# Optimization experiments

Hardware: AMD Instinct MI355X
Metric: run time of the kernel (lower is better)

Reference implementation:

```python
import jax, jax.numpy as jnp
import numpy as np

NUM_GROUPS = 8


def setup_inputs() -> dict:
    key = jax.random.key(0)
    k1, k2, k3, k4 = jax.random.split(key, 4)
    N, D_IN, D_OUT = 16384, 2048, 2048
    x = jax.random.normal(k1, (N, D_IN), dtype=jnp.float32)
    # kaiming-uniform-ish scale for weight, uniform bound for bias (values only need realistic scale)
    bound_w = 1.0 / np.sqrt(D_IN)
    weight = jax.random.uniform(k2, (NUM_GROUPS, D_OUT, D_IN), minval=-bound_w, maxval=bound_w, dtype=jnp.float32)
    bias = jax.random.uniform(k3, (NUM_GROUPS, D_OUT), minval=-bound_w, maxval=bound_w, dtype=jnp.float32)
    group_indices = jnp.sort(jax.random.randint(k4, (N,), 0, NUM_GROUPS, dtype=jnp.int32))
    return {"x": x, "weight": weight, "bias": bias, "group_indices": group_indices}


def reference(x, weight, bias, group_indices):
    """Grouped linear: out[n] = x[n] @ weight[g[n]].T + bias[g[n]].

    group_indices is sorted, so this matches the torch fallback's
    per-group gather + linear + concat row order exactly.
    """
    num_groups = weight.shape[0]
    out = jnp.zeros((x.shape[0], weight.shape[1]), dtype=x.dtype)
    for g in range(num_groups):  # fixed small loop over experts
        sel = (group_indices == g)[:, None]  # [N,1]
        # one dense GEMM per group, masked accumulate (rows not in group contribute 0)
        yg = jnp.matmul(x, weight[g].T) + bias[g]
        out = out + jnp.where(sel, yg, jnp.zeros((), dtype=x.dtype))
    return out
```

## Files before the change

kernel.cpp:

```cpp
#include <hip/hip_runtime.h>
#include <stdint.h>

#define N_ROWS 16384
#define K_DIM  2048
#define N_OUT  2048
#define NGROUPS 8
#define BM 128
#define BN 128
#define BK 32
#define MAX_Y 136

typedef short s16x8 __attribute__((ext_vector_type(8)));
typedef float f32x4 __attribute__((ext_vector_type(4)));

__device__ __forceinline__ unsigned short f2bf(float f) {
    unsigned int u = __float_as_uint(f);
    u += 0x7fffu + ((u >> 16) & 1u);
    return (unsigned short)(u >> 16);
}

__global__ void convert_kernel(const float* __restrict__ src,
                               unsigned short* __restrict__ dst, int n) {
    int stride = gridDim.x * blockDim.x;
    for (int i = blockIdx.x * blockDim.x + threadIdx.x; i * 4 < n; i += stride) {
        float4 v = *(const float4*)(src + (size_t)i * 4);
        ushort4 o;
        o.x = f2bf(v.x); o.y = f2bf(v.y); o.z = f2bf(v.z); o.w = f2bf(v.w);
        *(ushort4*)(dst + (size_t)i * 4) = o;
    }
}

__device__ __forceinline__ int lower_bound_g(const int* __restrict__ gi, int g) {
    int lo = 0, hi = N_ROWS;
    while (lo < hi) { int mid = (lo + hi) >> 1; if (gi[mid] < g) lo = mid + 1; else hi = mid; }
    return lo;
}

#define GLDS16(gp, lp) \
    __builtin_amdgcn_global_load_lds((__attribute__((address_space(1))) void*)(gp), \
                                     (__attribute__((address_space(3))) void*)(lp), 16, 0, 0)

__global__ __launch_bounds__(256) void grouped_gemm(
    const unsigned short* __restrict__ xb,
    const unsigned short* __restrict__ wb,
    const float* __restrict__ bias,
    const int* __restrict__ gi,
    float* __restrict__ out)
{
    int s[NGROUPS + 1];
    s[0] = 0; s[NGROUPS] = N_ROWS;
    #pragma unroll
    for (int g = 1; g < NGROUPS; g++) s[g] = lower_bound_g(gi, g);

    int by = blockIdx.y;
    int row0 = -1, g = 0, nrows = 0, c = 0;
    #pragma unroll
    for (int gg = 0; gg < NGROUPS; gg++) {
        int n = s[gg + 1] - s[gg];
        int tiles = (n + BM - 1) / BM;
        if (row0 < 0 && by < c + tiles) {
            g = gg;
            row0 = s[gg] + (by - c) * BM;
            nrows = n - (by - c) * BM; if (nrows > BM) nrows = BM;
        }
        c += tiles;
    }
    if (row0 < 0) return;
    int col0 = blockIdx.x * BN;

    __shared__ unsigned short As[BM * BK];
    __shared__ unsigned short Bs[BN * BK];

    int t = threadIdx.x;
    int w = t >> 6, l = t & 63;
    int la = l & 15, quad = l >> 4;
    int wm = w >> 1, wn = w & 1;

    int arow = w * 16 + (l >> 2);
    int kcol = (l & 3) * 8;
    int ar0 = min(row0 + arow,      N_ROWS - 1);
    int ar1 = min(row0 + 64 + arow, N_ROWS - 1);
    const unsigned short* gA0 = xb + (size_t)ar0 * K_DIM + kcol;
    const unsigned short* gA1 = xb + (size_t)ar1 * K_DIM + kcol;
    const unsigned short* gB0 = wb + ((size_t)g * N_OUT + col0 + arow) * K_DIM + kcol;
    const unsigned short* gB1 = gB0 + (size_t)64 * K_DIM;
    unsigned short* lA = As + w * 512;
    unsigned short* lB = Bs + w * 512;

    f32x4 acc[4][4];
    #pragma unroll
    for (int i = 0; i < 4; i++)
        #pragma unroll
        for (int j = 0; j < 4; j++)
            acc[i][j] = (f32x4){0.f, 0.f, 0.f, 0.f};

    for (int k0 = 0; k0 < K_DIM; k0 += BK) {
        GLDS16(gA0 + k0, lA);
        GLDS16(gA1 + k0, lA + 2048);
        GLDS16(gB0 + k0, lB);
        GLDS16(gB1 + k0, lB + 2048);
        __syncthreads();

        s16x8 af[4], bf_[4];
        #pragma unroll
        for (int mi = 0; mi < 4; mi++)
            af[mi] = *(const s16x8*)&As[(wm * 64 + mi * 16 + la) * BK + quad * 8];
        #pragma unroll
        for (int ni = 0; ni < 4; ni++)
            bf_[ni] = *(const s16x8*)&Bs[(wn * 64 + ni * 16 + la) * BK + quad * 8];

        #pragma unroll
        for (int mi = 0; mi < 4; mi++)
            #pragma unroll
            for (int ni = 0; ni < 4; ni++)
                acc[mi][ni] = __builtin_amdgcn_mfma_f32_16x16x32_bf16(
                    af[mi], bf_[ni], acc[mi][ni], 0, 0, 0);
        __syncthreads();
    }

    int row_end = row0 + nrows;
    float bv[4];
    #pragma unroll
    for (int ni = 0; ni < 4; ni++)
        bv[ni] = bias[g * N_OUT + col0 + wn * 64 + ni * 16 + la];
    #pragma unroll
    for (int mi = 0; mi < 4; mi++) {
        int rbase = row0 + wm * 64 + mi * 16 + quad * 4;
        #pragma unroll
        for (int r = 0; r < 4; r++) {
            int row = rbase + r;
            if (row < row_end) {
                float* op = out + (size_t)row * N_OUT + col0 + wn * 64 + la;
                #pragma unroll
                for (int ni = 0; ni < 4; ni++)
                    op[ni * 16] = acc[mi][ni][r] + bv[ni];
            }
        }
    }
}

__global__ void naive_kernel(const float* __restrict__ x, const float* __restrict__ wgt,
                             const float* __restrict__ bias, const int* __restrict__ gi,
                             float* __restrict__ out) {
    int row = blockIdx.x;
    int g = gi[row] & (NGROUPS - 1);
    __shared__ float xs[K_DIM];
    for (int i = threadIdx.x; i < K_DIM; i += 256) xs[i] = x[(size_t)row * K_DIM + i];
    __syncthreads();
    for (int c = threadIdx.x; c < N_OUT; c += 256) {
        const float* wr = wgt + ((size_t)g * N_OUT + c) * K_DIM;
        float s = 0.f;
        for (int k = 0; k < K_DIM; k++) s += xs[k] * wr[k];
        out[(size_t)row * N_OUT + c] = s + bias[g * N_OUT + c];
    }
}

extern "C" void kernel_launch(void* const* d_in, const int* in_sizes, int n_in,
                              void* d_out, int out_size, void* d_ws, size_t ws_size,
                              hipStream_t stream) {
    const float* x    = (const float*)d_in[0];
    const float* wgt  = (const float*)d_in[1];
    const float* bias = (const float*)d_in[2];
    const int*   gi   = (const int*)d_in[3];
    float* out = (float*)d_out;

    const size_t xb_bytes = (size_t)N_ROWS * K_DIM * 2;
    const size_t wb_bytes = (size_t)NGROUPS * N_OUT * K_DIM * 2;
    const size_t need = xb_bytes + wb_bytes;

    if (ws_size < need) {
        naive_kernel<<<dim3(N_ROWS), dim3(256), 0, stream>>>(x, wgt, bias, gi, out);
        return;
    }

    unsigned short* xb = (unsigned short*)d_ws;
    unsigned short* wb = (unsigned short*)((char*)d_ws + xb_bytes);

    convert_kernel<<<dim3(8192), dim3(256), 0, stream>>>(x,   xb, N_ROWS * K_DIM);
    convert_kernel<<<dim3(8192), dim3(256), 0, stream>>>(wgt, wb, NGROUPS * N_OUT * K_DIM);
    grouped_gemm<<<dim3(N_OUT / BN, MAX_Y), dim3(256), 0, stream>>>(
        xb, wb, bias, gi, out);
}
```

Baseline: 525.9 us.

## Rewrite grouped GEMM with 256x256x64 tiles, double-buffered swizzled LDS pipeline

```diff
diff --git a/kernel.cpp b/kernel.cpp
--- a/kernel.cpp
+++ b/kernel.cpp
@@ -5,10 +5,10 @@
 #define K_DIM  2048
 #define N_OUT  2048
 #define NGROUPS 8
-#define BM 128
-#define BN 128
-#define BK 32
-#define MAX_Y 136
+#define BM 256
+#define BN 256
+#define BK 64
+#define MAX_Y 72
 
 typedef short s16x8 __attribute__((ext_vector_type(8)));
 typedef float f32x4 __attribute__((ext_vector_type(4)));
@@ -40,27 +40,36 @@
     __builtin_amdgcn_global_load_lds((__attribute__((address_space(1))) void*)(gp), \
                                      (__attribute__((address_space(3))) void*)(lp), 16, 0, 0)
 
-__global__ __launch_bounds__(256) void grouped_gemm(
+#define VMW(N)  asm volatile("s_waitcnt vmcnt(" #N ")" ::: "memory")
+#define BAR()   asm volatile("s_barrier" ::: "memory")
+#define LGKM0() do { asm volatile("s_waitcnt lgkmcnt(0)" ::: "memory"); \
+                     __builtin_amdgcn_sched_barrier(0); } while (0)
+
+__global__ __launch_bounds__(512, 2) void grouped_gemm(
     const unsigned short* __restrict__ xb,
     const unsigned short* __restrict__ wb,
     const float* __restrict__ bias,
     const int* __restrict__ gi,
     float* __restrict__ out)
 {
-    int s[NGROUPS + 1];
-    s[0] = 0; s[NGROUPS] = N_ROWS;
-    #pragma unroll
-    for (int g = 1; g < NGROUPS; g++) s[g] = lower_bound_g(gi, g);
+    __shared__ unsigned char lds[131072];
+    __shared__ int sh_s[NGROUPS + 1];
+
+    const int t5 = threadIdx.x;
+
+    if (t5 <= NGROUPS)
+        sh_s[t5] = (t5 == 0) ? 0 : (t5 == NGROUPS ? N_ROWS : lower_bound_g(gi, t5));
+    __syncthreads();
 
     int by = blockIdx.y;
     int row0 = -1, g = 0, nrows = 0, c = 0;
     #pragma unroll
     for (int gg = 0; gg < NGROUPS; gg++) {
-        int n = s[gg + 1] - s[gg];
-        int tiles = (n + BM - 1) / BM;
+        int n = sh_s[gg + 1] - sh_s[gg];
+        int tiles = (n + BM - 1) >> 8;
         if (row0 < 0 && by < c + tiles) {
             g = gg;
-            row0 = s[gg] + (by - c) * BM;
+            row0 = sh_s[gg] + (by - c) * BM;
             nrows = n - (by - c) * BM; if (nrows > BM) nrows = BM;
         }
         c += tiles;
@@ -68,55 +77,80 @@
     if (row0 < 0) return;
     int col0 = blockIdx.x * BN;
 
-    __shared__ unsigned short As[BM * BK];
-    __shared__ unsigned short Bs[BN * BK];
-
-    int t = threadIdx.x;
-    int w = t >> 6, l = t & 63;
-    int la = l & 15, quad = l >> 4;
-    int wm = w >> 1, wn = w & 1;
-
-    int arow = w * 16 + (l >> 2);
-    int kcol = (l & 3) * 8;
-    int ar0 = min(row0 + arow,      N_ROWS - 1);
-    int ar1 = min(row0 + 64 + arow, N_ROWS - 1);
-    const unsigned short* gA0 = xb + (size_t)ar0 * K_DIM + kcol;
-    const unsigned short* gA1 = xb + (size_t)ar1 * K_DIM + kcol;
-    const unsigned short* gB0 = wb + ((size_t)g * N_OUT + col0 + arow) * K_DIM + kcol;
-    const unsigned short* gB1 = gB0 + (size_t)64 * K_DIM;
-    unsigned short* lA = As + w * 512;
-    unsigned short* lB = Bs + w * 512;
-
-    f32x4 acc[4][4];
-    #pragma unroll
-    for (int i = 0; i < 4; i++)
+    int rsub = t5 >> 2;
+    int swz  = (t5 & 3) ^ ((rsub >> 1) & 3);
+    int ar0 = min(row0 + rsub,       N_ROWS - 1);
+    int ar1 = min(row0 + 128 + rsub, N_ROWS - 1);
+    const unsigned short* srcA0 = xb + (size_t)ar0 * K_DIM + swz * 8;
+    const unsigned short* srcA1 = xb + (size_t)ar1 * K_DIM + swz * 8;
+    const unsigned short* srcB0 = wb + ((size_t)g * N_OUT + col0 + rsub) * K_DIM + swz * 8;
+    const unsigned short* srcB1 = srcB0 + (size_t)128 * K_DIM;
+    char* ldsA = (char*)lds;
+    char* ldsB = (char*)lds + 65536;
+    char* dA = ldsA + t5 * 16;
+    char* dB = ldsB + t5 * 16;
+
+#define STAGE_A(BUF,H,KT) do { \
+    GLDS16(srcA0 + (KT)*64 + (H)*32, dA + (BUF)*32768 + (H)*16384); \
+    GLDS16(srcA1 + (KT)*64 + (H)*32, dA + (BUF)*32768 + (H)*16384 + 8192); } while (0)
+#define STAGE_B(BUF,H,KT) do { \
+    GLDS16(srcB0 + (KT)*64 + (H)*32, dB + (BUF)*32768 + (H)*16384); \
+    GLDS16(srcB1 + (KT)*64 + (H)*32, dB + (BUF)*32768 + (H)*16384 + 8192); } while (0)
+
+    int w = t5 >> 6, l = t5 & 63, la = l & 15, q = l >> 4;
+    int wm = w >> 2, wn = w & 3;
+    int swr   = (q ^ ((la >> 1) & 3)) * 16;
+    int aOff0 = (wm * 128 + la) * 64 + swr;
+    int bOff0 = (wn * 64  + la) * 64 + swr;
+
+#define RDA8(DST, BUF, KS) do { _Pragma("unroll") \
+    for (int mi = 0; mi < 8; mi++) \
+        DST[mi] = *(const s16x8*)(ldsA + (BUF)*32768 + (KS)*16384 + aOff0 + mi*1024); } while (0)
+#define RDB1(DST, BUF, KS, NI) \
+    DST = *(const s16x8*)(ldsB + (BUF)*32768 + (KS)*16384 + bOff0 + (NI)*1024)
+
+    f32x4 acc[8][4];
+    #pragma unroll
+    for (int i2 = 0; i2 < 8; i2++)
         #pragma unroll
-        for (int j = 0; j < 4; j++)
-            acc[i][j] = (f32x4){0.f, 0.f, 0.f, 0.f};
-
-    for (int k0 = 0; k0 < K_DIM; k0 += BK) {
-        GLDS16(gA0 + k0, lA);
-        GLDS16(gA1 + k0, lA + 2048);
-        GLDS16(gB0 + k0, lB);
-        GLDS16(gB1 + k0, lB + 2048);
-        __syncthreads();
-
-        s16x8 af[4], bf_[4];
-        #pragma unroll
-        for (int mi = 0; mi < 4; mi++)
-            af[mi] = *(const s16x8*)&As[(wm * 64 + mi * 16 + la) * BK + quad * 8];
-        #pragma unroll
-        for (int ni = 0; ni < 4; ni++)
-            bf_[ni] = *(const s16x8*)&Bs[(wn * 64 + ni * 16 + la) * BK + quad * 8];
-
-        #pragma unroll
-        for (int mi = 0; mi < 4; mi++)
-            #pragma unroll
-            for (int ni = 0; ni < 4; ni++)
-                acc[mi][ni] = __builtin_amdgcn_mfma_f32_16x16x32_bf16(
-                    af[mi], bf_[ni], acc[mi][ni], 0, 0, 0);
-        __syncthreads();
-    }
+        for (int j2 = 0; j2 < 4; j2++)
+            acc[i2][j2] = (f32x4){0.f, 0.f, 0.f, 0.f};
+
+    s16x8 a0[8], a1[8], b0[4], b1[4];
+
+#define MFMA16(AF, BL, BH, N0, N1) do { \
+    __builtin_amdgcn_s_setprio(1); \
+    _Pragma("unroll") for (int mi = 0; mi < 8; mi++) { \
+        acc[mi][N0] = __builtin_amdgcn_mfma_f32_16x16x32_bf16(AF[mi], BL, acc[mi][N0], 0, 0, 0); \
+        acc[mi][N1] = __builtin_amdgcn_mfma_f32_16x16x32_bf16(AF[mi], BH, acc[mi][N1], 0, 0, 0); } \
+    __builtin_amdgcn_s_setprio(0); } while (0)
+
+#define QTILE(BUF, ST1, ST2, ST3, ST4, W4) do { \
+    RDA8(a0, BUF, 0); RDB1(b0[0], BUF, 0, 0); RDB1(b0[1], BUF, 0, 1); \
+    ST1; BAR(); LGKM0(); MFMA16(a0, b0[0], b0[1], 0, 1); BAR(); \
+    RDB1(b0[2], BUF, 0, 2); RDB1(b0[3], BUF, 0, 3); \
+    ST2; BAR(); LGKM0(); MFMA16(a0, b0[2], b0[3], 2, 3); BAR(); \
+    RDA8(a1, BUF, 1); RDB1(b1[0], BUF, 1, 0); RDB1(b1[1], BUF, 1, 1); \
+    ST3; BAR(); LGKM0(); MFMA16(a1, b1[0], b1[1], 0, 1); BAR(); \
+    RDB1(b1[2], BUF, 1, 2); RDB1(b1[3], BUF, 1, 3); \
+    ST4; W4; BAR(); LGKM0(); MFMA16(a1, b1[2], b1[3], 2, 3); BAR(); \
+} while (0)
+
+    STAGE_A(0,0,0); STAGE_B(0,0,0); STAGE_A(0,1,0); STAGE_B(0,1,0);
+    STAGE_A(1,0,1); STAGE_B(1,0,1); STAGE_A(1,1,1);
+    VMW(6);
+    BAR();
+
+    #pragma unroll 1
+    for (int i = 0; i < 15; i++) {
+        int kt0 = 2 * i + 2, kt1 = 2 * i + 3, ktp = 2 * i + 1;
+        QTILE(0, STAGE_B(1,1,ktp), STAGE_A(0,0,kt0), STAGE_B(0,0,kt0),
+                 STAGE_A(0,1,kt0), VMW(6));
+        QTILE(1, STAGE_B(0,1,kt0), STAGE_A(1,0,kt1), STAGE_B(1,0,kt1),
+                 STAGE_A(1,1,kt1), VMW(6));
+    }
+    QTILE(0, STAGE_B(1,1,31), ((void)0), ((void)0), ((void)0), VMW(0));
+    QTILE(1, ((void)0), ((void)0), ((void)0), ((void)0), ((void)0));
 
     int row_end = row0 + nrows;
     float bv[4];
@@ -124,8 +158,8 @@
     for (int ni = 0; ni < 4; ni++)
         bv[ni] = bias[g * N_OUT + col0 + wn * 64 + ni * 16 + la];
     #pragma unroll
-    for (int mi = 0; mi < 4; mi++) {
-        int rbase = row0 + wm * 64 + mi * 16 + quad * 4;
+    for (int mi = 0; mi < 8; mi++) {
+        int rbase = row0 + wm * 128 + mi * 16 + q * 4;
         #pragma unroll
         for (int r = 0; r < 4; r++) {
             int row = rbase + r;
@@ -178,6 +212,6 @@
 
     convert_kernel<<<dim3(8192), dim3(256), 0, stream>>>(x,   xb, N_ROWS * K_DIM);
     convert_kernel<<<dim3(8192), dim3(256), 0, stream>>>(wgt, wb, NGROUPS * N_OUT * K_DIM);
-    grouped_gemm<<<dim3(N_OUT / BN, MAX_Y), dim3(256), 0, stream>>>(
+    grouped_gemm<<<dim3(N_OUT / BN, MAX_Y), dim3(512), 0, stream>>>(
         xb, wb, bias, gi, out);
 }
```

Result: faster. 494.4 us (-6.0%).
